# Performance work log

Measured on AMD Instinct MI355X. Metric: run time of the kernel, lower is better.

## Reference

```python
import jax, jax.numpy as jnp
import numpy as np

N_NODES = 50000
N_EDGES = 800000
IN_CH = 128
HID = 64   # 2 * out_channels
OUT = 32   # out_channels
SLOPE = 0.2  # PyG GATConv default negative_slope


def _gat_layer(x, W, a_src, a_dst, b, src, dst):
    """Single-head GATConv: proj -> edge attention logits -> segment softmax
    over destination nodes -> scatter-aggregate weighted source messages."""
    n = x.shape[0]
    h = x @ W                                   # [N, C]
    ls = h @ a_src                              # [N] per-node src score
    ld = h @ a_dst                              # [N] per-node dst score
    logits = jax.nn.leaky_relu(ls[src] + ld[dst], negative_slope=SLOPE)  # [E]
    # numerically stable segment softmax grouped by destination node
    lmax = jax.ops.segment_max(logits, dst, num_segments=n)              # [N]
    e = jnp.exp(logits - lmax[dst])                                      # [E]
    denom = jax.ops.segment_sum(e, dst, num_segments=n)                  # [N]
    alpha = e / denom[dst]                                               # [E]
    out = jax.ops.segment_sum(alpha[:, None] * h[src], dst, num_segments=n)
    return out + b


def setup_inputs() -> dict:
    key = jax.random.key(0)
    ks = jax.random.split(key, 10)
    x = jax.random.normal(ks[0], (N_NODES, IN_CH), dtype=jnp.float32)
    edge_index = jax.random.randint(ks[1], (2, N_EDGES), 0, N_NODES, dtype=jnp.int32)
    s1 = 1.0 / np.sqrt(IN_CH)
    s2 = 1.0 / np.sqrt(HID)
    return {
        "x": x,
        "edge_index": edge_index,
        "W1": jax.random.normal(ks[2], (IN_CH, HID), dtype=jnp.float32) * s1,
        "a_src1": jax.random.normal(ks[3], (HID,), dtype=jnp.float32) * s2,
        "a_dst1": jax.random.normal(ks[4], (HID,), dtype=jnp.float32) * s2,
        "b1": jnp.zeros((HID,), dtype=jnp.float32),
        "W2": jax.random.normal(ks[5], (HID, OUT), dtype=jnp.float32) * s2,
        "a_src2": jax.random.normal(ks[6], (OUT,), dtype=jnp.float32) / np.sqrt(OUT),
        "a_dst2": jax.random.normal(ks[7], (OUT,), dtype=jnp.float32) / np.sqrt(OUT),
        "b2": jnp.zeros((OUT,), dtype=jnp.float32),
    }


def reference(x, edge_index, W1, a_src1, a_dst1, b1, W2, a_src2, a_dst2, b2):
    src, dst = edge_index[0], edge_index[1]
    h = jax.nn.relu(_gat_layer(x, W1, a_src1, a_dst1, b1, src, dst))
    return _gat_layer(h, W2, a_src2, a_dst2, b2, src, dst)
```

## Files before the change

### kernel.cpp

```cpp
#include <hip/hip_runtime.h>
#include <hip/hip_fp16.h>


#define N_NODES 50000
#define N_EDGES 800000
#define SLOPE 0.2f
#define NBUCK 196
#define CAP 4608

typedef _Float16 half4 __attribute__((ext_vector_type(4)));

__global__ __launch_bounds__(256) void k_zerobins(int* __restrict__ binctr)
{
    if (threadIdx.x < NBUCK) binctr[threadIdx.x] = 0;
}

__global__ __launch_bounds__(1024) void k_bin(
    const int* __restrict__ src, const int* __restrict__ dst,
    int* __restrict__ binctr, int* __restrict__ stg)
{
    __shared__ int hist[NBUCK];
    __shared__ int gb[NBUCK];
    const int t = threadIdx.x;
    if (t < NBUCK) hist[t] = 0;
    __syncthreads();

    const int base = blockIdx.x * 4096;
    int mp[4], mb[4], mr[4];
    int n = 0;
    #pragma unroll
    for (int k = 0; k < 4; ++k) {
        int e = base + t + k * 1024;
        if (e < N_EDGES) {
            int s = src[e], d = dst[e];
            int b = d >> 8;
            mp[n] = s | ((d & 255) << 16);
            mb[n] = b;
            mr[n] = atomicAdd(&hist[b], 1);
            ++n;
        }
    }
    __syncthreads();
    if (t < NBUCK) gb[t] = atomicAdd(&binctr[t], hist[t]);
    __syncthreads();
    for (int i = 0; i < n; ++i)
        stg[mb[i] * CAP + gb[mb[i]] + mr[i]] = mp[i];
}

__global__ __launch_bounds__(256) void k_btot(
    const int* __restrict__ binctr, int* __restrict__ bucket_base)
{
    __shared__ int tmp[256];
    const int t = threadIdx.x;
    int v = (t < NBUCK) ? binctr[t] : 0;
    tmp[t] = v;
    __syncthreads();
    #pragma unroll
    for (int off = 1; off < 256; off <<= 1) {
        int u = (t >= off) ? tmp[t - off] : 0;
        __syncthreads();
        tmp[t] += u;
        __syncthreads();
    }
    if (t < NBUCK) bucket_base[t] = tmp[t] - v;
}

__global__ __launch_bounds__(1024) void k_sort(
    const int* __restrict__ stg,
    const int* __restrict__ binctr, const int* __restrict__ bucket_base,
    int* __restrict__ row_start, int* __restrict__ csr_src)
{
    __shared__ int cnt[256];
    __shared__ int off[256];
    const int b = blockIdx.x, t = threadIdx.x;
    const int n = binctr[b];
    const int sbase = b * CAP;
    const int obase = bucket_base[b];

    if (t < 256) cnt[t] = 0;
    __syncthreads();

    int mv[5], mk[5], mr[5];
    int c = 0;
    for (int i = t; i < n; i += 1024) {
        int v = stg[sbase + i];
        int k = v >> 16;
        mv[c] = v & 0xFFFF;
        mk[c] = k;
        mr[c] = atomicAdd(&cnt[k], 1);
        ++c;
    }
    __syncthreads();

    if (t < 256) off[t] = cnt[t];
    __syncthreads();
    #pragma unroll
    for (int o = 1; o < 256; o <<= 1) {
        int u = (t < 256 && t >= o) ? off[t - o] : 0;
        __syncthreads();
        if (t < 256) off[t] += u;
        __syncthreads();
    }

    if (t < 256) {
        int node = b * 256 + t;
        if (node < N_NODES) row_start[node] = obase + off[t] - cnt[t];
    }
    if (b == NBUCK - 1 && t == 0) row_start[N_NODES] = N_EDGES;

    for (int i = 0; i < c; ++i)
        csr_src[obase + off[mk[i]] - cnt[mk[i]] + mr[i]] = mv[i];
}

__global__ __launch_bounds__(256) void k_gemm1(
    const float* __restrict__ x, const float* __restrict__ W1,
    const float* __restrict__ a_src, const float* __restrict__ a_dst,
    _Float16* __restrict__ h1h, float* __restrict__ ls, float* __restrict__ ld)
{
    __shared__ float As[64][128];
    __shared__ float Bs[128][64];
    const int tid = threadIdx.x;
    const int m0 = blockIdx.x * 64;

    {
        const float4* Wv = (const float4*)W1;
        float4* Bv = (float4*)&Bs[0][0];
        #pragma unroll
        for (int i = 0; i < 8; ++i) Bv[tid + i * 256] = Wv[tid + i * 256];
    }
    {
        const float4* Xv = (const float4*)x;
        #pragma unroll
        for (int i = 0; i < 8; ++i) {
            int idx = tid + i * 256;
            int r = idx >> 5, kq = idx & 31;
            float4 v = make_float4(0.f, 0.f, 0.f, 0.f);
            if (m0 + r < N_NODES) v = Xv[(size_t)(m0 + r) * 32 + kq];
            ((float4*)&As[r][0])[kq] = v;
        }
    }
    __syncthreads();

    const int tx = tid & 15, ty = tid >> 4;
    const int c0 = tx * 4, r0 = ty * 4;
    float acc[4][4] = {};
    for (int k = 0; k < 128; k += 4) {
        float a_s[4][4];
        #pragma unroll
        for (int i = 0; i < 4; ++i) {
            float4 av = *(const float4*)&As[r0 + i][k];
            a_s[i][0] = av.x; a_s[i][1] = av.y; a_s[i][2] = av.z; a_s[i][3] = av.w;
        }
        #pragma unroll
        for (int kk = 0; kk < 4; ++kk) {
            float4 b = *(const float4*)&Bs[k + kk][c0];
            #pragma unroll
            for (int i = 0; i < 4; ++i) {
                acc[i][0] += a_s[i][kk] * b.x;
                acc[i][1] += a_s[i][kk] * b.y;
                acc[i][2] += a_s[i][kk] * b.z;
                acc[i][3] += a_s[i][kk] * b.w;
            }
        }
    }

    float as4[4], ad4[4];
    #pragma unroll
    for (int j = 0; j < 4; ++j) { as4[j] = a_src[c0 + j]; ad4[j] = a_dst[c0 + j]; }

    #pragma unroll
    for (int i = 0; i < 4; ++i) {
        int row = m0 + r0 + i;
        float pls = acc[i][0]*as4[0] + acc[i][1]*as4[1] + acc[i][2]*as4[2] + acc[i][3]*as4[3];
        float pld = acc[i][0]*ad4[0] + acc[i][1]*ad4[1] + acc[i][2]*ad4[2] + acc[i][3]*ad4[3];
        #pragma unroll
        for (int off = 1; off < 16; off <<= 1) {
            pls += __shfl_xor(pls, off, 64);
            pld += __shfl_xor(pld, off, 64);
        }
        if (row < N_NODES) {
            half4 hv;
            hv.x = (_Float16)acc[i][0]; hv.y = (_Float16)acc[i][1];
            hv.z = (_Float16)acc[i][2]; hv.w = (_Float16)acc[i][3];
            ((half4*)&h1h[(size_t)row * 64])[tx] = hv;
            if (tx == 0) { ls[row] = pls; ld[row] = pld; }
        }
    }
}

__global__ __launch_bounds__(256) void k_agg1(
    const int* __restrict__ csr_src, const int* __restrict__ row_start,
    const float* __restrict__ ls, const float* __restrict__ ld,
    const _Float16* __restrict__ h1h, const float* __restrict__ b1,
    float* __restrict__ acc1)
{
    const int node = blockIdx.x * 4 + (threadIdx.x >> 6);
    const int lane = threadIdx.x & 63;
    const int c4 = lane & 15, eslot = lane >> 4;
    const int beg = row_start[node], end = row_start[node + 1];
    const float ldv = ld[node];
    const half4* H = (const half4*)h1h;

    float4 acc = make_float4(0.f, 0.f, 0.f, 0.f);
    float sw = 0.f;
    for (int base = beg; base < end; base += 64) {
        const int cnt = min(64, end - base);
        int s = 0;
        float w = 0.f;
        if (lane < cnt) {
            s = csr_src[base + lane];
            float l = ls[s] + ldv;
            l = l > 0.f ? l : SLOPE * l;
            w = __expf(l);
        }
        float wsum = w;
        #pragma unroll
        for (int off = 1; off < 64; off <<= 1) wsum += __shfl_xor(wsum, off, 64);
        sw += wsum;

        int j = 0;
        for (; j + 8 <= cnt; j += 8) {
            int   s0 = __shfl(s, j + eslot, 64);
            int   s1 = __shfl(s, j + 4 + eslot, 64);
            float w0 = __shfl(w, j + eslot, 64);
            float w1 = __shfl(w, j + 4 + eslot, 64);
            half4 g0 = H[(size_t)s0 * 16 + c4];
            half4 g1 = H[(size_t)s1 * 16 + c4];
            acc.x += w0 * (float)g0.x; acc.y += w0 * (float)g0.y;
            acc.z += w0 * (float)g0.z; acc.w += w0 * (float)g0.w;
            acc.x += w1 * (float)g1.x; acc.y += w1 * (float)g1.y;
            acc.z += w1 * (float)g1.z; acc.w += w1 * (float)g1.w;
        }
        for (; j < cnt; j += 4) {
            int   sj = __shfl(s, j + eslot, 64);
            float wj = __shfl(w, j + eslot, 64);
            half4 g = H[(size_t)sj * 16 + c4];
            acc.x += wj * (float)g.x; acc.y += wj * (float)g.y;
            acc.z += wj * (float)g.z; acc.w += wj * (float)g.w;
        }
    }
    #pragma unroll
    for (int off = 16; off < 64; off <<= 1) {
        acc.x += __shfl_xor(acc.x, off, 64);
        acc.y += __shfl_xor(acc.y, off, 64);
        acc.z += __shfl_xor(acc.z, off, 64);
        acc.w += __shfl_xor(acc.w, off, 64);
    }
    if (eslot == 0) {
        float inv = sw > 0.f ? 1.f / sw : 0.f;
        float4 bb = ((const float4*)b1)[c4];
        ((float4*)&acc1[(size_t)node * 64])[c4] =
            make_float4(acc.x * inv + bb.x, acc.y * inv + bb.y,
                        acc.z * inv + bb.z, acc.w * inv + bb.w);
    }
}

__global__ __launch_bounds__(256) void k_epi1(
    const float* __restrict__ acc1, const float* __restrict__ W2,
    const float* __restrict__ a_src2, const float* __restrict__ a_dst2,
    _Float16* __restrict__ h2h, float* __restrict__ ls2, float* __restrict__ ld2)
{
    __shared__ float Hs[64][68];
    __shared__ float W2s[64][32];
    const int tid = threadIdx.x;
    const int n0 = blockIdx.x * 64;

    {
        const float4* Wv = (const float4*)W2;
        float4* Ws = (float4*)&W2s[0][0];
        Ws[tid] = Wv[tid];
        Ws[tid + 256] = Wv[tid + 256];
    }
    {
        const float4* Av = (const float4*)acc1;
        #pragma unroll
        for (int i = 0; i < 4; ++i) {
            int idx = tid + i * 256;
            int r = idx >> 4, kq = idx & 15;
            float4 v = make_float4(0.f, 0.f, 0.f, 0.f);
            if (n0 + r < N_NODES) {
                v = Av[(size_t)(n0 + r) * 16 + kq];
                v.x = fmaxf(v.x, 0.f); v.y = fmaxf(v.y, 0.f);
                v.z = fmaxf(v.z, 0.f); v.w = fmaxf(v.w, 0.f);
            }
            ((float4*)&Hs[r][0])[kq] = v;
        }
    }
    __syncthreads();

    const int nl = tid >> 2, cg = tid & 3, c0 = cg * 8;
    float acc[8] = {};
    for (int k4 = 0; k4 < 16; ++k4) {
        float4 hv4 = *(const float4*)&Hs[nl][k4 * 4];
        #pragma unroll
        for (int kk = 0; kk < 4; ++kk) {
            float hv = kk == 0 ? hv4.x : kk == 1 ? hv4.y : kk == 2 ? hv4.z : hv4.w;
            int k = k4 * 4 + kk;
            float4 w0 = *(const float4*)&W2s[k][c0];
            float4 w1 = *(const float4*)&W2s[k][c0 + 4];
            acc[0] += hv * w0.x; acc[1] += hv * w0.y;
            acc[2] += hv * w0.z; acc[3] += hv * w0.w;
            acc[4] += hv * w1.x; acc[5] += hv * w1.y;
            acc[6] += hv * w1.z; acc[7] += hv * w1.w;
        }
    }

    float pls = 0.f, pld = 0.f;
    #pragma unroll
    for (int j = 0; j < 8; ++j) {
        pls += acc[j] * a_src2[c0 + j];
        pld += acc[j] * a_dst2[c0 + j];
    }
    pls += __shfl_xor(pls, 1, 64); pls += __shfl_xor(pls, 2, 64);
    pld += __shfl_xor(pld, 1, 64); pld += __shfl_xor(pld, 2, 64);

    int node = n0 + nl;
    if (node < N_NODES) {
        half4 lo, hi;
        lo.x = (_Float16)acc[0]; lo.y = (_Float16)acc[1];
        lo.z = (_Float16)acc[2]; lo.w = (_Float16)acc[3];
        hi.x = (_Float16)acc[4]; hi.y = (_Float16)acc[5];
        hi.z = (_Float16)acc[6]; hi.w = (_Float16)acc[7];
        ((half4*)&h2h[(size_t)node * 32])[cg * 2]     = lo;
        ((half4*)&h2h[(size_t)node * 32])[cg * 2 + 1] = hi;
        if (cg == 0) { ls2[node] = pls; ld2[node] = pld; }
    }
}

__global__ __launch_bounds__(256) void k_agg2(
    const int* __restrict__ csr_src, const int* __restrict__ row_start,
    const float* __restrict__ ls, const float* __restrict__ ld,
    const _Float16* __restrict__ h2h, const float* __restrict__ b2,
    float* __restrict__ out)
{
    const int idx = blockIdx.x * 256 + threadIdx.x;
    const int node = idx >> 5;
    const int grp = idx & 31;
    const int c4 = grp & 7, eslot = grp >> 3;
    const int beg = row_start[node], end = row_start[node + 1];
    const float ldv = ld[node];
    const half4* H = (const half4*)h2h;

    float4 acc = make_float4(0.f, 0.f, 0.f, 0.f);
    float sw = 0.f;
    for (int base = beg; base < end; base += 32) {
        const int cnt = min(32, end - base);
        int s = 0;
        float w = 0.f;
        if (grp < cnt) {
            s = csr_src[base + grp];
            float l = ls[s] + ldv;
            l = l > 0.f ? l : SLOPE * l;
            w = __expf(l);
        }
        float wsum = w;
        #pragma unroll
        for (int off = 1; off < 32; off <<= 1) wsum += __shfl_xor(wsum, off, 32);
        sw += wsum;

        int j = 0;
        for (; j + 8 <= cnt; j += 8) {
            int   s0 = __shfl(s, j + eslot, 32);
            int   s1 = __shfl(s, j + 4 + eslot, 32);
            float w0 = __shfl(w, j + eslot, 32);
            float w1 = __shfl(w, j + 4 + eslot, 32);
            half4 g0 = H[(size_t)s0 * 8 + c4];
            half4 g1 = H[(size_t)s1 * 8 + c4];
            acc.x += w0 * (float)g0.x; acc.y += w0 * (float)g0.y;
            acc.z += w0 * (float)g0.z; acc.w += w0 * (float)g0.w;
            acc.x += w1 * (float)g1.x; acc.y += w1 * (float)g1.y;
            acc.z += w1 * (float)g1.z; acc.w += w1 * (float)g1.w;
        }
        for (; j < cnt; j += 4) {
            int   sj = __shfl(s, j + eslot, 32);
            float wj = __shfl(w, j + eslot, 32);
            half4 g = H[(size_t)sj * 8 + c4];
            acc.x += wj * (float)g.x; acc.y += wj * (float)g.y;
            acc.z += wj * (float)g.z; acc.w += wj * (float)g.w;
        }
    }
    #pragma unroll
    for (int off = 8; off < 32; off <<= 1) {
        acc.x += __shfl_xor(acc.x, off, 32);
        acc.y += __shfl_xor(acc.y, off, 32);
        acc.z += __shfl_xor(acc.z, off, 32);
        acc.w += __shfl_xor(acc.w, off, 32);
    }
    if (eslot == 0) {
        float inv = sw > 0.f ? 1.f / sw : 0.f;
        float4 bb = ((const float4*)b2)[c4];
        ((float4*)&out[(size_t)node * 32])[c4] =
            make_float4(acc.x * inv + bb.x, acc.y * inv + bb.y,
                        acc.z * inv + bb.z, acc.w * inv + bb.w);
    }
}

extern "C" void kernel_launch(void* const* d_in, const int* in_sizes, int n_in,
                              void* d_out, int out_size, void* d_ws, size_t ws_size,
                              hipStream_t stream)
{
    const float* x      = (const float*)d_in[0];
    const int*   ei     = (const int*)  d_in[1];
    const float* W1     = (const float*)d_in[2];
    const float* a_src1 = (const float*)d_in[3];
    const float* a_dst1 = (const float*)d_in[4];
    const float* b1     = (const float*)d_in[5];
    const float* W2     = (const float*)d_in[6];
    const float* a_src2 = (const float*)d_in[7];
    const float* a_dst2 = (const float*)d_in[8];
    const float* b2     = (const float*)d_in[9];
    const int* src = ei;
    const int* dst = ei + N_EDGES;
    float* out = (float*)d_out;

    float* ws   = (float*)d_ws;
    _Float16* h1h = (_Float16*)ws;
    float* acc1 = ws + 1600000;
    float* ls1  = ws + 4800000;
    float* ld1  = ws + 4850000;
    int* row_start   = (int*)(ws + 4900000);
    int* csr_src     = (int*)(ws + 4950016);
    int* binctr      = (int*)(ws + 5750016);
    int* bucket_base = (int*)(ws + 5750272);
    int* stg = (int*)ws;
    _Float16* h2h = h1h;
    float* ls2 = ls1;
    float* ld2 = ld1;

    k_zerobins<<<1,   256,  0, stream>>>(binctr);
    k_bin     <<<196, 1024, 0, stream>>>(src, dst, binctr, stg);
    k_btot    <<<1,   256,  0, stream>>>(binctr, bucket_base);
    k_sort    <<<NBUCK, 1024, 0, stream>>>(stg, binctr, bucket_base,
                                           row_start, csr_src);

    k_gemm1<<<782,   256, 0, stream>>>(x, W1, a_src1, a_dst1, h1h, ls1, ld1);
    k_agg1 <<<12500, 256, 0, stream>>>(csr_src, row_start, ls1, ld1, h1h, b1, acc1);

    k_epi1 <<<782,  256, 0, stream>>>(acc1, W2, a_src2, a_dst2, h2h, ls2, ld2);
    k_agg2 <<<6250, 256, 0, stream>>>(csr_src, row_start, ls2, ld2, h2h, b2, out);
}
```

Measured before the change: 181.5 us.

## Fuse edge binning with layer-1 GEMM, fold bucket scan into sort, use 16-bit CSR

Edge binning and the first projection GEMM now run in one launch, split by block index, so the two independent stages can overlap and one launch disappears. The bucket prefix scan moves into each sort block, which removes the separate scan kernel at the cost of every block repeating a small redundant scan. CSR source indices are stored as 16-bit values, halving index traffic in both aggregation kernels; this relies on node ids staying below 65536. The staging buffer moves to its own workspace region so it no longer aliases h1h while the GEMM writes it.

```diff
diff --git a/kernel.cpp b/kernel.cpp
--- a/kernel.cpp
+++ b/kernel.cpp
@@ -7,6 +7,8 @@
 #define SLOPE 0.2f
 #define NBUCK 196
 #define CAP 4608
+#define BIN_BLOCKS 196
+#define GEMM_BLOCKS 782
 
 typedef _Float16 half4 __attribute__((ext_vector_type(4)));
 
@@ -15,70 +17,135 @@
     if (threadIdx.x < NBUCK) binctr[threadIdx.x] = 0;
 }
 
-__global__ __launch_bounds__(1024) void k_bin(
+__global__ __launch_bounds__(256) void k_pre(
     const int* __restrict__ src, const int* __restrict__ dst,
-    int* __restrict__ binctr, int* __restrict__ stg)
-{
+    int* __restrict__ binctr, int* __restrict__ stg,
+    const float* __restrict__ x, const float* __restrict__ W1,
+    const float* __restrict__ a_src, const float* __restrict__ a_dst,
+    _Float16* __restrict__ h1h, float* __restrict__ ls, float* __restrict__ ld)
+{
+    __shared__ float As[64][128];
+    __shared__ float Bs[128][64];
     __shared__ int hist[NBUCK];
     __shared__ int gb[NBUCK];
-    const int t = threadIdx.x;
-    if (t < NBUCK) hist[t] = 0;
+    const int tid = threadIdx.x;
+
+    if (blockIdx.x < BIN_BLOCKS) {
+        if (tid < NBUCK) hist[tid] = 0;
+        __syncthreads();
+
+        const int base = blockIdx.x * 4096;
+        int ms[16], md[16], mr[16];
+        #pragma unroll
+        for (int k = 0; k < 16; ++k) {
+            int e = base + tid + k * 256;
+            int s = 0, d = 0;
+            if (e < N_EDGES) { s = src[e]; d = dst[e]; }
+            ms[k] = s; md[k] = d;
+            mr[k] = (e < N_EDGES) ? atomicAdd(&hist[d >> 8], 1) : -1;
+        }
+        __syncthreads();
+        if (tid < NBUCK) gb[tid] = atomicAdd(&binctr[tid], hist[tid]);
+        __syncthreads();
+        #pragma unroll
+        for (int k = 0; k < 16; ++k) {
+            if (mr[k] >= 0) {
+                int b = md[k] >> 8;
+                stg[b * CAP + gb[b] + mr[k]] = ms[k] | ((md[k] & 255) << 16);
+            }
+        }
+        return;
+    }
+
+    const int m0 = (blockIdx.x - BIN_BLOCKS) * 64;
+
+    {
+        const float4* Wv = (const float4*)W1;
+        float4* Bv = (float4*)&Bs[0][0];
+        #pragma unroll
+        for (int i = 0; i < 8; ++i) Bv[tid + i * 256] = Wv[tid + i * 256];
+    }
+    {
+        const float4* Xv = (const float4*)x;
+        #pragma unroll
+        for (int i = 0; i < 8; ++i) {
+            int idx = tid + i * 256;
+            int r = idx >> 5, kq = idx & 31;
+            float4 v = make_float4(0.f, 0.f, 0.f, 0.f);
+            if (m0 + r < N_NODES) v = Xv[(size_t)(m0 + r) * 32 + kq];
+            ((float4*)&As[r][0])[kq] = v;
+        }
+    }
     __syncthreads();
 
-    const int base = blockIdx.x * 4096;
-    int mp[4], mb[4], mr[4];
-    int n = 0;
-    #pragma unroll
-    for (int k = 0; k < 4; ++k) {
-        int e = base + t + k * 1024;
-        if (e < N_EDGES) {
-            int s = src[e], d = dst[e];
-            int b = d >> 8;
-            mp[n] = s | ((d & 255) << 16);
-            mb[n] = b;
-            mr[n] = atomicAdd(&hist[b], 1);
-            ++n;
-        }
-    }
-    __syncthreads();
-    if (t < NBUCK) gb[t] = atomicAdd(&binctr[t], hist[t]);
-    __syncthreads();
-    for (int i = 0; i < n; ++i)
-        stg[mb[i] * CAP + gb[mb[i]] + mr[i]] = mp[i];
-}
-
-__global__ __launch_bounds__(256) void k_btot(
-    const int* __restrict__ binctr, int* __restrict__ bucket_base)
-{
-    __shared__ int tmp[256];
-    const int t = threadIdx.x;
-    int v = (t < NBUCK) ? binctr[t] : 0;
-    tmp[t] = v;
-    __syncthreads();
-    #pragma unroll
-    for (int off = 1; off < 256; off <<= 1) {
-        int u = (t >= off) ? tmp[t - off] : 0;
-        __syncthreads();
-        tmp[t] += u;
-        __syncthreads();
-    }
-    if (t < NBUCK) bucket_base[t] = tmp[t] - v;
+    const int tx = tid & 15, ty = tid >> 4;
+    const int c0 = tx * 4, r0 = ty * 4;
+    float acc[4][4] = {};
+    for (int k = 0; k < 128; k += 4) {
+        float a_s[4][4];
+        #pragma unroll
+        for (int i = 0; i < 4; ++i) {
+            float4 av = *(const float4*)&As[r0 + i][k];
+            a_s[i][0] = av.x; a_s[i][1] = av.y; a_s[i][2] = av.z; a_s[i][3] = av.w;
+        }
+        #pragma unroll
+        for (int kk = 0; kk < 4; ++kk) {
+            float4 b = *(const float4*)&Bs[k + kk][c0];
+            #pragma unroll
+            for (int i = 0; i < 4; ++i) {
+                acc[i][0] += a_s[i][kk] * b.x;
+                acc[i][1] += a_s[i][kk] * b.y;
+                acc[i][2] += a_s[i][kk] * b.z;
+                acc[i][3] += a_s[i][kk] * b.w;
+            }
+        }
+    }
+
+    float as4[4], ad4[4];
+    #pragma unroll
+    for (int j = 0; j < 4; ++j) { as4[j] = a_src[c0 + j]; ad4[j] = a_dst[c0 + j]; }
+
+    #pragma unroll
+    for (int i = 0; i < 4; ++i) {
+        int row = m0 + r0 + i;
+        float pls = acc[i][0]*as4[0] + acc[i][1]*as4[1] + acc[i][2]*as4[2] + acc[i][3]*as4[3];
+        float pld = acc[i][0]*ad4[0] + acc[i][1]*ad4[1] + acc[i][2]*ad4[2] + acc[i][3]*ad4[3];
+        #pragma unroll
+        for (int off = 1; off < 16; off <<= 1) {
+            pls += __shfl_xor(pls, off, 64);
+            pld += __shfl_xor(pld, off, 64);
+        }
+        if (row < N_NODES) {
+            half4 hv;
+            hv.x = (_Float16)acc[i][0]; hv.y = (_Float16)acc[i][1];
+            hv.z = (_Float16)acc[i][2]; hv.w = (_Float16)acc[i][3];
+            ((half4*)&h1h[(size_t)row * 64])[tx] = hv;
+            if (tx == 0) { ls[row] = pls; ld[row] = pld; }
+        }
+    }
 }
 
 __global__ __launch_bounds__(1024) void k_sort(
-    const int* __restrict__ stg,
-    const int* __restrict__ binctr, const int* __restrict__ bucket_base,
-    int* __restrict__ row_start, int* __restrict__ csr_src)
+    const int* __restrict__ stg, const int* __restrict__ binctr,
+    int* __restrict__ row_start, unsigned short* __restrict__ csr_src)
 {
     __shared__ int cnt[256];
     __shared__ int off[256];
+    __shared__ int sc[256];
     const int b = blockIdx.x, t = threadIdx.x;
     const int n = binctr[b];
     const int sbase = b * CAP;
-    const int obase = bucket_base[b];
-
-    if (t < 256) cnt[t] = 0;
+
+    if (t < 256) { sc[t] = (t < NBUCK) ? binctr[t] : 0; cnt[t] = 0; }
     __syncthreads();
+    #pragma unroll
+    for (int o = 1; o < 256; o <<= 1) {
+        int u = (t < 256 && t >= o) ? sc[t - o] : 0;
+        __syncthreads();
+        if (t < 256) sc[t] += u;
+        __syncthreads();
+    }
+    const int obase = sc[b] - n;
 
     int mv[5], mk[5], mr[5];
     int c = 0;
@@ -109,87 +176,11 @@
     if (b == NBUCK - 1 && t == 0) row_start[N_NODES] = N_EDGES;
 
     for (int i = 0; i < c; ++i)
-        csr_src[obase + off[mk[i]] - cnt[mk[i]] + mr[i]] = mv[i];
-}
-
-__global__ __launch_bounds__(256) void k_gemm1(
-    const float* __restrict__ x, const float* __restrict__ W1,
-    const float* __restrict__ a_src, const float* __restrict__ a_dst,
-    _Float16* __restrict__ h1h, float* __restrict__ ls, float* __restrict__ ld)
-{
-    __shared__ float As[64][128];
-    __shared__ float Bs[128][64];
-    const int tid = threadIdx.x;
-    const int m0 = blockIdx.x * 64;
-
-    {
-        const float4* Wv = (const float4*)W1;
-        float4* Bv = (float4*)&Bs[0][0];
-        #pragma unroll
-        for (int i = 0; i < 8; ++i) Bv[tid + i * 256] = Wv[tid + i * 256];
-    }
-    {
-        const float4* Xv = (const float4*)x;
-        #pragma unroll
-        for (int i = 0; i < 8; ++i) {
-            int idx = tid + i * 256;
-            int r = idx >> 5, kq = idx & 31;
-            float4 v = make_float4(0.f, 0.f, 0.f, 0.f);
-            if (m0 + r < N_NODES) v = Xv[(size_t)(m0 + r) * 32 + kq];
-            ((float4*)&As[r][0])[kq] = v;
-        }
-    }
-    __syncthreads();
-
-    const int tx = tid & 15, ty = tid >> 4;
-    const int c0 = tx * 4, r0 = ty * 4;
-    float acc[4][4] = {};
-    for (int k = 0; k < 128; k += 4) {
-        float a_s[4][4];
-        #pragma unroll
-        for (int i = 0; i < 4; ++i) {
-            float4 av = *(const float4*)&As[r0 + i][k];
-            a_s[i][0] = av.x; a_s[i][1] = av.y; a_s[i][2] = av.z; a_s[i][3] = av.w;
-        }
-        #pragma unroll
-        for (int kk = 0; kk < 4; ++kk) {
-            float4 b = *(const float4*)&Bs[k + kk][c0];
-            #pragma unroll
-            for (int i = 0; i < 4; ++i) {
-                acc[i][0] += a_s[i][kk] * b.x;
-                acc[i][1] += a_s[i][kk] * b.y;
-                acc[i][2] += a_s[i][kk] * b.z;
-                acc[i][3] += a_s[i][kk] * b.w;
-            }
-        }
-    }
-
-    float as4[4], ad4[4];
-    #pragma unroll
-    for (int j = 0; j < 4; ++j) { as4[j] = a_src[c0 + j]; ad4[j] = a_dst[c0 + j]; }
-
-    #pragma unroll
-    for (int i = 0; i < 4; ++i) {
-        int row = m0 + r0 + i;
-        float pls = acc[i][0]*as4[0] + acc[i][1]*as4[1] + acc[i][2]*as4[2] + acc[i][3]*as4[3];
-        float pld = acc[i][0]*ad4[0] + acc[i][1]*ad4[1] + acc[i][2]*ad4[2] + acc[i][3]*ad4[3];
-        #pragma unroll
-        for (int off = 1; off < 16; off <<= 1) {
-            pls += __shfl_xor(pls, off, 64);
-            pld += __shfl_xor(pld, off, 64);
-        }
-        if (row < N_NODES) {
-            half4 hv;
-            hv.x = (_Float16)acc[i][0]; hv.y = (_Float16)acc[i][1];
-            hv.z = (_Float16)acc[i][2]; hv.w = (_Float16)acc[i][3];
-            ((half4*)&h1h[(size_t)row * 64])[tx] = hv;
-            if (tx == 0) { ls[row] = pls; ld[row] = pld; }
-        }
-    }
+        csr_src[obase + off[mk[i]] - cnt[mk[i]] + mr[i]] = (unsigned short)mv[i];
 }
 
 __global__ __launch_bounds__(256) void k_agg1(
-    const int* __restrict__ csr_src, const int* __restrict__ row_start,
+    const unsigned short* __restrict__ csr_src, const int* __restrict__ row_start,
     const float* __restrict__ ls, const float* __restrict__ ld,
     const _Float16* __restrict__ h1h, const float* __restrict__ b1,
     float* __restrict__ acc1)
@@ -328,7 +319,7 @@
 }
 
 __global__ __launch_bounds__(256) void k_agg2(
-    const int* __restrict__ csr_src, const int* __restrict__ row_start,
+    const unsigned short* __restrict__ csr_src, const int* __restrict__ row_start,
     const float* __restrict__ ls, const float* __restrict__ ld,
     const _Float16* __restrict__ h2h, const float* __restrict__ b2,
     float* __restrict__ out)
@@ -418,24 +409,19 @@
     float* acc1 = ws + 1600000;
     float* ls1  = ws + 4800000;
     float* ld1  = ws + 4850000;
-    int* row_start   = (int*)(ws + 4900000);
-    int* csr_src     = (int*)(ws + 4950016);
-    int* binctr      = (int*)(ws + 5750016);
-    int* bucket_base = (int*)(ws + 5750272);
-    int* stg = (int*)ws;
+    int* row_start = (int*)(ws + 4900000);
+    unsigned short* csr16 = (unsigned short*)(ws + 4950016);
+    int* binctr = (int*)(ws + 5350032);
+    int* stg    = (int*)(ws + 5350288);
     _Float16* h2h = h1h;
     float* ls2 = ls1;
     float* ld2 = ld1;
 
-    k_zerobins<<<1,   256,  0, stream>>>(binctr);
-    k_bin     <<<196, 1024, 0, stream>>>(src, dst, binctr, stg);
-    k_btot    <<<1,   256,  0, stream>>>(binctr, bucket_base);
-    k_sort    <<<NBUCK, 1024, 0, stream>>>(stg, binctr, bucket_base,
-                                           row_start, csr_src);
-
-    k_gemm1<<<782,   256, 0, stream>>>(x, W1, a_src1, a_dst1, h1h, ls1, ld1);
-    k_agg1 <<<12500, 256, 0, stream>>>(csr_src, row_start, ls1, ld1, h1h, b1, acc1);
-
+    k_zerobins<<<1, 256, 0, stream>>>(binctr);
+    k_pre  <<<BIN_BLOCKS + GEMM_BLOCKS, 256, 0, stream>>>(
+        src, dst, binctr, stg, x, W1, a_src1, a_dst1, h1h, ls1, ld1);
+    k_sort <<<NBUCK, 1024, 0, stream>>>(stg, binctr, row_start, csr16);
+    k_agg1 <<<12500, 256, 0, stream>>>(csr16, row_start, ls1, ld1, h1h, b1, acc1);
     k_epi1 <<<782,  256, 0, stream>>>(acc1, W2, a_src2, a_dst2, h2h, ls2, ld2);
-    k_agg2 <<<6250, 256, 0, stream>>>(csr_src, row_start, ls2, ld2, h2h, b2, out);
-}
+    k_agg2 <<<6250, 256, 0, stream>>>(csr16, row_start, ls2, ld2, h2h, b2, out);
+}
```

Measured after the change: 169.5 us (median of 2 runs). -6.6%, faster.
